# Optimization experiments

Hardware: AMD Instinct MI355X
Metric: run time of the kernel (lower is better)

Reference implementation:

```python
import jax, jax.numpy as jnp
import numpy as np

T, H, D = 32768, 32, 128   # total packed tokens, heads, head_dim
ROPE_DIM = 64              # rotary channels (rest pass through)
MAX_SEQLEN = 4096


def setup_inputs() -> dict:
    key = jax.random.key(0)
    k1, k2, k3 = jax.random.split(key, 3)
    # 16 ragged sequences, lengths alternating 1024/3072 (sum = 32768, all <= MAX_SEQLEN)
    lengths = np.array([1024, 3072] * 8, dtype=np.int64)
    cu = np.concatenate([[0], np.cumsum(lengths)]).astype(np.int32)  # [17]
    return {
        "input": jax.random.normal(k1, (T, H, D), jnp.float32),
        "sin_cache": jax.random.uniform(k2, (MAX_SEQLEN, ROPE_DIM), jnp.float32, -1.0, 1.0),
        "cos_cache": jax.random.uniform(k3, (MAX_SEQLEN, ROPE_DIM), jnp.float32, -1.0, 1.0),
        "cu_seqlen": jnp.asarray(cu),
        "max_seqlen": MAX_SEQLEN,
    }


def reference(input, sin_cache, cos_cache, cu_seqlen, max_seqlen):
    # Packed ragged RoPE, interleaved=False, position_id=None (per-seq positions
    # restart at 0), dynamic=False. Vectorized over all tokens at once.
    rope_dim = sin_cache.shape[-1]
    total = input.shape[0]
    tok = jnp.arange(total)
    # segment id of each packed token, then its offset within its sequence
    seg = jnp.searchsorted(cu_seqlen, tok, side="right") - 1          # [T]
    off = tok - cu_seqlen[seg]                                        # [T]
    sin = sin_cache[off]                                              # [T, rope_dim]
    cos = cos_cache[off]                                              # [T, rope_dim]
    x = input[..., :rope_dim]                                         # [T, H, rope_dim]
    x1, x2 = jnp.split(x, 2, axis=-1)
    rot = jnp.concatenate((-x2, x1), axis=-1)                         # rotate halves
    out_rope = rot * sin[:, None, :] + x * cos[:, None, :]
    return jnp.concatenate((out_rope, input[..., rope_dim:]), axis=-1)
```

## Files before the change

kernel.cpp:

```cpp
#include <hip/hip_runtime.h>
#include <limits.h>

#define NUM_HEADS 32
#define HEAD_DIM 128
#define ROPE_DIM 64

typedef float v4f __attribute__((ext_vector_type(4)));

__global__ __launch_bounds__(256) void ApplyRotary_27814208209209_kernel(
    const float* __restrict__ in,
    const float* __restrict__ sin_cache,
    const float* __restrict__ cos_cache,
    const int* __restrict__ cu_seqlen,
    int n_cu,
    float* __restrict__ out)
{
    const int t   = blockIdx.x;
    const int tid = threadIdx.x;
    const int lane = tid & 63;

    int off;
    if (n_cu <= 64) {
        const int cuv = (lane < n_cu) ? cu_seqlen[lane] : INT_MAX;
        const unsigned long long le = __ballot(cuv <= t);
        const int seg = __popcll(le) - 1;
        off = t - __shfl(cuv, seg);
    } else {
        int seg = 0;
        while (seg + 1 < n_cu && cu_seqlen[seg + 1] <= t) seg++;
        off = t - cu_seqlen[seg];
    }

    const v4f* in4  = (const v4f*)(in  + (size_t)t * NUM_HEADS * HEAD_DIM);
    v4f*       out4 = (v4f*)      (out + (size_t)t * NUM_HEADS * HEAD_DIM);
    const v4f* sin4 = (const v4f*)(sin_cache + (size_t)off * ROPE_DIM);
    const v4f* cos4 = (const v4f*)(cos_cache + (size_t)off * ROPE_DIM);

    {
        const int h = tid >> 3;
        const int p = tid & 7;
        const int base = h * (HEAD_DIM / 4);

        const v4f a = __builtin_nontemporal_load(&in4[base + p]);
        const v4f b = __builtin_nontemporal_load(&in4[base + p + 8]);

        const v4f s1 = sin4[p];
        const v4f c1 = cos4[p];
        const v4f s2 = sin4[p + 8];
        const v4f c2 = cos4[p + 8];

        v4f oa, ob;
        oa.x = fmaf(-b.x, s1.x, a.x * c1.x);
        oa.y = fmaf(-b.y, s1.y, a.y * c1.y);
        oa.z = fmaf(-b.z, s1.z, a.z * c1.z);
        oa.w = fmaf(-b.w, s1.w, a.w * c1.w);
        ob.x = fmaf(a.x, s2.x, b.x * c2.x);
        ob.y = fmaf(a.y, s2.y, b.y * c2.y);
        ob.z = fmaf(a.z, s2.z, b.z * c2.z);
        ob.w = fmaf(a.w, s2.w, b.w * c2.w);

        __builtin_nontemporal_store(oa, &out4[base + p]);
        __builtin_nontemporal_store(ob, &out4[base + p + 8]);
    }

    #pragma unroll
    for (int j = tid; j < NUM_HEADS * (HEAD_DIM - ROPE_DIM) / 4; j += 256) {
        const int h = j >> 4;
        const int q = j & 15;
        const int idx = h * (HEAD_DIM / 4) + (ROPE_DIM / 4) + q;
        const v4f v = __builtin_nontemporal_load(&in4[idx]);
        __builtin_nontemporal_store(v, &out4[idx]);
    }
}

extern "C" void kernel_launch(void* const* d_in, const int* in_sizes, int n_in,
                              void* d_out, int out_size, void* d_ws, size_t ws_size,
                              hipStream_t stream) {
    const float* in        = (const float*)d_in[0];
    const float* sin_cache = (const float*)d_in[1];
    const float* cos_cache = (const float*)d_in[2];
    const int*   cu        = (const int*)d_in[3];
    const int    n_cu      = in_sizes[3];

    const int total_tokens = in_sizes[0] / (NUM_HEADS * HEAD_DIM);

    ApplyRotary_27814208209209_kernel<<<total_tokens, 256, 0, stream>>>(
        in, sin_cache, cos_cache, cu, n_cu, (float*)d_out);
}
```

Baseline: 817.6 us.

## Use persistent grid-stride blocks with hoisted segment lookup and early loads

Measured after the change: 822.2 us. No clear change (+0.6%).

```diff
diff --git a/kernel.cpp b/kernel.cpp
--- a/kernel.cpp
+++ b/kernel.cpp
@@ -13,37 +13,38 @@
     const float* __restrict__ cos_cache,
     const int* __restrict__ cu_seqlen,
     int n_cu,
+    int total_tokens,
     float* __restrict__ out)
 {
-    const int t   = blockIdx.x;
-    const int tid = threadIdx.x;
+    const int tid  = threadIdx.x;
     const int lane = tid & 63;
 
-    int off;
-    if (n_cu <= 64) {
-        const int cuv = (lane < n_cu) ? cu_seqlen[lane] : INT_MAX;
+    const int cuv = (lane < n_cu) ? cu_seqlen[lane] : INT_MAX;
+
+    const int h = tid >> 3;
+    const int p = tid & 7;
+    const int ropeBase = h * (HEAD_DIM / 4);
+
+    const int j0 = tid;
+    const int j1 = tid + 256;
+    const int idx0 = (j0 >> 4) * (HEAD_DIM / 4) + (ROPE_DIM / 4) + (j0 & 15);
+    const int idx1 = (j1 >> 4) * (HEAD_DIM / 4) + (ROPE_DIM / 4) + (j1 & 15);
+
+    for (int t = blockIdx.x; t < total_tokens; t += gridDim.x) {
+        const v4f* in4  = (const v4f*)(in  + (size_t)t * (NUM_HEADS * HEAD_DIM));
+        v4f*       out4 = (v4f*)      (out + (size_t)t * (NUM_HEADS * HEAD_DIM));
+
+        const v4f a  = __builtin_nontemporal_load(&in4[ropeBase + p]);
+        const v4f b  = __builtin_nontemporal_load(&in4[ropeBase + p + 8]);
+        const v4f v0 = __builtin_nontemporal_load(&in4[idx0]);
+        const v4f v1 = __builtin_nontemporal_load(&in4[idx1]);
+
         const unsigned long long le = __ballot(cuv <= t);
         const int seg = __popcll(le) - 1;
-        off = t - __shfl(cuv, seg);
-    } else {
-        int seg = 0;
-        while (seg + 1 < n_cu && cu_seqlen[seg + 1] <= t) seg++;
-        off = t - cu_seqlen[seg];
-    }
+        const int off = t - __shfl(cuv, seg);
 
-    const v4f* in4  = (const v4f*)(in  + (size_t)t * NUM_HEADS * HEAD_DIM);
-    v4f*       out4 = (v4f*)      (out + (size_t)t * NUM_HEADS * HEAD_DIM);
-    const v4f* sin4 = (const v4f*)(sin_cache + (size_t)off * ROPE_DIM);
-    const v4f* cos4 = (const v4f*)(cos_cache + (size_t)off * ROPE_DIM);
-
-    {
-        const int h = tid >> 3;
-        const int p = tid & 7;
-        const int base = h * (HEAD_DIM / 4);
-
-        const v4f a = __builtin_nontemporal_load(&in4[base + p]);
-        const v4f b = __builtin_nontemporal_load(&in4[base + p + 8]);
-
+        const v4f* sin4 = (const v4f*)(sin_cache + (size_t)off * ROPE_DIM);
+        const v4f* cos4 = (const v4f*)(cos_cache + (size_t)off * ROPE_DIM);
         const v4f s1 = sin4[p];
         const v4f c1 = cos4[p];
         const v4f s2 = sin4[p + 8];
@@ -59,17 +60,10 @@
         ob.z = fmaf(a.z, s2.z, b.z * c2.z);
         ob.w = fmaf(a.w, s2.w, b.w * c2.w);
 
-        __builtin_nontemporal_store(oa, &out4[base + p]);
-        __builtin_nontemporal_store(ob, &out4[base + p + 8]);
-    }
-
-    #pragma unroll
-    for (int j = tid; j < NUM_HEADS * (HEAD_DIM - ROPE_DIM) / 4; j += 256) {
-        const int h = j >> 4;
-        const int q = j & 15;
-        const int idx = h * (HEAD_DIM / 4) + (ROPE_DIM / 4) + q;
-        const v4f v = __builtin_nontemporal_load(&in4[idx]);
-        __builtin_nontemporal_store(v, &out4[idx]);
+        __builtin_nontemporal_store(oa, &out4[ropeBase + p]);
+        __builtin_nontemporal_store(ob, &out4[ropeBase + p + 8]);
+        __builtin_nontemporal_store(v0, &out4[idx0]);
+        __builtin_nontemporal_store(v1, &out4[idx1]);
     }
 }
 
@@ -84,6 +78,8 @@
 
     const int total_tokens = in_sizes[0] / (NUM_HEADS * HEAD_DIM);
 
-    ApplyRotary_27814208209209_kernel<<<total_tokens, 256, 0, stream>>>(
-        in, sin_cache, cos_cache, cu, n_cu, (float*)d_out);
+    int blocks = total_tokens < 2048 ? total_tokens : 2048;
+
+    ApplyRotary_27814208209209_kernel<<<blocks, 256, 0, stream>>>(
+        in, sin_cache, cos_cache, cu, n_cu, total_tokens, (float*)d_out);
 }
```
